# Performance work log

Hardware: AMD Instinct MI355X
Metric: run time of the kernel (lower is better)

Reference implementation:

```python
import jax, jax.numpy as jnp
import numpy as np

S, E, H, V = 2048, 1024, 1024, 32000


def setup_inputs() -> dict:
    key = jax.random.key(0)
    ks = jax.random.split(key, 12)
    def n(k, shape, s=0.02):
        return jax.random.normal(k, shape, dtype=jnp.float32) * s
    return {
        "encoder_out": n(ks[0], (S, E), 1.0),
        "word_input": jax.random.randint(ks[1], (1,), 0, V),
        "last_context": n(ks[2], (1, H), 1.0),
        "h0": jnp.zeros((1, 1, H), jnp.float32),
        "c0": jnp.zeros((1, 1, H), jnp.float32),
        "emb": n(ks[3], (V, E)),
        "W_ih": n(ks[4], (4 * H, E + H)),
        "b_ih": jnp.zeros((4 * H,), jnp.float32),
        "W_hh": n(ks[5], (4 * H, H)),
        "b_hh": jnp.zeros((4 * H,), jnp.float32),
        "W_att": n(ks[6], (H, E + H)),
        "b_att": jnp.zeros((H,), jnp.float32),
        "v": jax.random.uniform(ks[7], (H,), dtype=jnp.float32) * 0.1,
        "W_ah": n(ks[8], (H, E + H)),
        "b_ah": jnp.zeros((H,), jnp.float32),
        "W_out": n(ks[9], (V, H)),
        "b_out": jnp.zeros((V,), jnp.float32),
    }


def reference(encoder_out, word_input, last_context, h0, c0, emb,
              W_ih, b_ih, W_hh, b_hh, W_att, b_att, v, W_ah, b_ah,
              W_out, b_out):
    # --- single LSTM step (torch gate order: i, f, g, o) ---
    x_emb = emb[word_input[0]]                         # [E]
    lstm_in = jnp.concatenate([last_context[0], x_emb])  # [E+H]
    gates = W_ih @ lstm_in + b_ih + W_hh @ h0[0, 0] + b_hh  # [4H]
    i, f, g, o = jnp.split(gates, 4)
    i = jax.nn.sigmoid(i); f = jax.nn.sigmoid(f)
    g = jnp.tanh(g);       o = jax.nn.sigmoid(o)
    c = f * c0[0, 0] + i * g                           # [H]
    h = o * jnp.tanh(c)                                # [H] (dropout: eval = identity)

    # --- batched additive (Bahdanau-style) attention over all S steps ---
    cat = jnp.concatenate([jnp.broadcast_to(h[None, :], (S, H)), encoder_out], axis=1)  # [S, H+E]
    scores = jnp.tanh(cat @ W_att.T + b_att) @ v       # [S]
    w = jax.nn.softmax(scores)                         # [S]
    context = w @ encoder_out                          # [E]

    # --- output projection ---
    x_t = jnp.tanh(W_ah @ jnp.concatenate([context, h]) + b_ah)  # [H]
    output = jax.nn.log_softmax(W_out @ x_t + b_out)[None, :]    # [1, V]
    return (output, (h[None, None, :], c[None, None, :]), x_t[None, :], w[None, :])
```

## Files before the change

### kernel.cpp

```cpp
#include <hip/hip_runtime.h>
#include <math.h>

typedef unsigned short u16;
typedef unsigned int u32;

typedef float  floatx4 __attribute__((ext_vector_type(4)));
typedef short  shortx8 __attribute__((ext_vector_type(8)));

#define S_LEN 2048
#define E_DIM 1024
#define H_DIM 1024
#define V_DIM 32000

#define OUT_LOG 0
#define OUT_H   32000
#define OUT_C   33024
#define OUT_XT  34048
#define OUT_W   35072

#define WS_UB     0
#define WS_SCORES 1024
#define WS_CTX    3072
#define WS_EXPSUM 4097

__device__ __forceinline__ u16 f2bf_fast(float f) {
    union { float f; u32 i; } v; v.f = f;
    return (u16)((v.i + 0x8000u) >> 16);
}
__device__ __forceinline__ float red16_sum(float x) {
    #pragma unroll
    for (int m = 1; m <= 8; m <<= 1) x += __shfl_xor(x, m, 64);
    return x;
}
__device__ __forceinline__ float wave_sum(float x) {
    #pragma unroll
    for (int m = 32; m >= 1; m >>= 1) x += __shfl_xor(x, m, 64);
    return x;
}
__device__ __forceinline__ float wave_max(float x) {
    #pragma unroll
    for (int m = 32; m >= 1; m >>= 1) x = fmaxf(x, __shfl_xor(x, m, 64));
    return x;
}
__device__ __forceinline__ float dot4(float4 a, float4 b) {
    return a.x * b.x + a.y * b.y + a.z * b.z + a.w * b.w;
}
__device__ __forceinline__ void cvt8(u16* t, float4 a, float4 b) {
    t[0] = f2bf_fast(a.x); t[1] = f2bf_fast(a.y);
    t[2] = f2bf_fast(a.z); t[3] = f2bf_fast(a.w);
    t[4] = f2bf_fast(b.x); t[5] = f2bf_fast(b.y);
    t[6] = f2bf_fast(b.z); t[7] = f2bf_fast(b.w);
}

__global__ __launch_bounds__(256) void k_lstm(
    const float* __restrict__ last_ctx, const int* __restrict__ word,
    const float* __restrict__ emb, const float* __restrict__ h0,
    const float* __restrict__ c0,
    const float* __restrict__ W_ih, const float* __restrict__ b_ih,
    const float* __restrict__ W_hh, const float* __restrict__ b_hh,
    float* __restrict__ out_h, float* __restrict__ out_c)
{
    __shared__ float gsh[4];
    int tid = threadIdx.x;
    int g = tid >> 6, l = tid & 63;
    int j = blockIdx.x;
    int row = g * H_DIM + j;
    const float* embrow = emb + (size_t)word[0] * E_DIM;
    const float* wrow = W_ih + (size_t)row * (E_DIM + H_DIM);
    const float* hrow = W_hh + (size_t)row * H_DIM;
    int c4 = l * 4;

    float s = 0.f;
    #pragma unroll
    for (int it = 0; it < 4; ++it) {
        int col = it * 256 + c4;
        s += dot4(*(const float4*)(wrow + col), *(const float4*)(last_ctx + col));
    }
    #pragma unroll
    for (int it = 0; it < 4; ++it) {
        int col = it * 256 + c4;
        s += dot4(*(const float4*)(wrow + 1024 + col), *(const float4*)(embrow + col));
    }
    #pragma unroll
    for (int it = 0; it < 4; ++it) {
        int col = it * 256 + c4;
        s += dot4(*(const float4*)(hrow + col), *(const float4*)(h0 + col));
    }
    s = wave_sum(s);
    if (l == 0) gsh[g] = s + b_ih[row] + b_hh[row];
    __syncthreads();
    if (tid == 0) {
        float gi = 1.f / (1.f + expf(-gsh[0]));
        float gf = 1.f / (1.f + expf(-gsh[1]));
        float gg = tanhf(gsh[2]);
        float go = 1.f / (1.f + expf(-gsh[3]));
        float c = gf * c0[j] + gi * gg;
        float h = go * tanhf(c);
        out_h[j] = h;
        out_c[j] = c;
    }
}

__global__ __launch_bounds__(256) void k_uproj(
    const float* __restrict__ W_att, const float* __restrict__ b_att,
    const float* __restrict__ out_h, float* __restrict__ wsf)
{
    int tid = threadIdx.x;
    int gid = blockIdx.x * 256 + tid;
    if (gid < S_LEN) wsf[WS_SCORES + gid] = 0.f;
    else if (gid < S_LEN + E_DIM) wsf[WS_CTX + gid - S_LEN] = 0.f;
    else if (gid == S_LEN + E_DIM) wsf[WS_EXPSUM] = 0.f;

    int w = tid >> 6, l = tid & 63;
    int r = blockIdx.x * 4 + w;
    const float* wrow = W_att + (size_t)r * (E_DIM + H_DIM);
    int c4 = l * 4;
    float s = 0.f;
    #pragma unroll
    for (int it = 0; it < 4; ++it) {
        int col = it * 256 + c4;
        s += dot4(*(const float4*)(wrow + col), *(const float4*)(out_h + col));
    }
    s = wave_sum(s);
    if (l == 0) wsf[WS_UB + r] = s + b_att[r];
}

#define LDS_P 40
__global__ __launch_bounds__(256) void k_att_scores(
    const float* __restrict__ enc, const float* __restrict__ W_att,
    const float* __restrict__ vvec, const float* __restrict__ ws_ub,
    float* __restrict__ ws_scores)
{
    __shared__ u16 lds_a[2][128 * LDS_P];
    __shared__ u16 lds_b[2][64 * LDS_P];

    int tid = threadIdx.x;
    int w = tid >> 6, l = tid & 63;
    int b = blockIdx.x;
    int s0 = (b & 15) * 128;
    int r0 = (b >> 4) * 64;
    int lrow = l & 15, lq = l >> 4;

    int arow = tid >> 1, acol = (tid & 1) * 16;
    int brow = tid >> 2, bcol = (tid & 3) * 8;
    const float* pa_base = enc + (size_t)(s0 + arow) * E_DIM + acol;
    const float* pb_base = W_att + (size_t)(r0 + brow) * (E_DIM + H_DIM) + H_DIM + bcol;

    floatx4 acc[2][4];
    #pragma unroll
    for (int sf = 0; sf < 2; ++sf)
        #pragma unroll
        for (int i = 0; i < 4; ++i) acc[sf][i] = (floatx4)0.f;

    {
        float4 a0 = *(const float4*)(pa_base);
        float4 a1 = *(const float4*)(pa_base + 4);
        float4 a2 = *(const float4*)(pa_base + 8);
        float4 a3 = *(const float4*)(pa_base + 12);
        float4 b0 = *(const float4*)(pb_base);
        float4 b1 = *(const float4*)(pb_base + 4);
        u16 t[16];
        cvt8(t, a0, a1); cvt8(t + 8, a2, a3);
        *(uint4*)&lds_a[0][arow * LDS_P + acol]     = *(uint4*)(t);
        *(uint4*)&lds_a[0][arow * LDS_P + acol + 8] = *(uint4*)(t + 8);
        u16 tb[8];
        cvt8(tb, b0, b1);
        *(uint4*)&lds_b[0][brow * LDS_P + bcol] = *(uint4*)(tb);
    }
    __syncthreads();

    int cur = 0;
    for (int kc = 0; kc < 32; ++kc) {
        float4 nA0, nA1, nA2, nA3, nB0, nB1;
        if (kc < 31) {
            const float* pa = pa_base + (kc + 1) * 32;
            nA0 = *(const float4*)(pa);
            nA1 = *(const float4*)(pa + 4);
            nA2 = *(const float4*)(pa + 8);
            nA3 = *(const float4*)(pa + 12);
            const float* pb = pb_base + (kc + 1) * 32;
            nB0 = *(const float4*)(pb);
            nB1 = *(const float4*)(pb + 4);
        }

        shortx8 afrag0 = *(const shortx8*)&lds_a[cur][(w * 32 + lrow) * LDS_P + lq * 8];
        shortx8 afrag1 = *(const shortx8*)&lds_a[cur][(w * 32 + 16 + lrow) * LDS_P + lq * 8];
        #pragma unroll
        for (int rc = 0; rc < 4; ++rc) {
            shortx8 bfrag = *(const shortx8*)&lds_b[cur][(rc * 16 + lrow) * LDS_P + lq * 8];
            acc[0][rc] = __builtin_amdgcn_mfma_f32_16x16x32_bf16(afrag0, bfrag, acc[0][rc], 0, 0, 0);
            acc[1][rc] = __builtin_amdgcn_mfma_f32_16x16x32_bf16(afrag1, bfrag, acc[1][rc], 0, 0, 0);
        }

        if (kc < 31) {
            int nb = cur ^ 1;
            u16 t[16];
            cvt8(t, nA0, nA1); cvt8(t + 8, nA2, nA3);
            *(uint4*)&lds_a[nb][arow * LDS_P + acol]     = *(uint4*)(t);
            *(uint4*)&lds_a[nb][arow * LDS_P + acol + 8] = *(uint4*)(t + 8);
            u16 tb[8];
            cvt8(tb, nB0, nB1);
            *(uint4*)&lds_b[nb][brow * LDS_P + bcol] = *(uint4*)(tb);
        }
        __syncthreads();
        cur ^= 1;
    }

    float part[2][4] = {{0.f,0.f,0.f,0.f},{0.f,0.f,0.f,0.f}};
    #pragma unroll
    for (int rc = 0; rc < 4; ++rc) {
        int r = r0 + rc * 16 + lrow;
        float ubr = ws_ub[r];
        float vr  = vvec[r];
        #pragma unroll
        for (int sf = 0; sf < 2; ++sf)
            #pragma unroll
            for (int reg = 0; reg < 4; ++reg)
                part[sf][reg] += tanhf(acc[sf][rc][reg] + ubr) * vr;
    }
    #pragma unroll
    for (int m = 1; m <= 8; m <<= 1)
        #pragma unroll
        for (int sf = 0; sf < 2; ++sf)
            #pragma unroll
            for (int reg = 0; reg < 4; ++reg)
                part[sf][reg] += __shfl_xor(part[sf][reg], m, 64);
    if (lrow == 0) {
        #pragma unroll
        for (int sf = 0; sf < 2; ++sf) {
            int sbase = s0 + w * 32 + sf * 16 + lq * 4;
            #pragma unroll
            for (int reg = 0; reg < 4; ++reg)
                atomicAdd(&ws_scores[sbase + reg], part[sf][reg]);
        }
    }
}

__global__ __launch_bounds__(256) void k_ctx(
    const float* __restrict__ enc, const float* __restrict__ ws_scores,
    float* __restrict__ out_w, float* __restrict__ ws_ctx)
{
    __shared__ float red[4];
    __shared__ float w_lds[16];
    __shared__ float bM, bS;
    int tid = threadIdx.x, b = blockIdx.x;

    float4 sa = *(const float4*)(ws_scores + tid * 8);
    float4 sb = *(const float4*)(ws_scores + tid * 8 + 4);
    float m = fmaxf(fmaxf(fmaxf(sa.x, sa.y), fmaxf(sa.z, sa.w)),
                    fmaxf(fmaxf(sb.x, sb.y), fmaxf(sb.z, sb.w)));
    m = wave_max(m);
    if ((tid & 63) == 0) red[tid >> 6] = m;
    __syncthreads();
    if (tid == 0) bM = fmaxf(fmaxf(red[0], red[1]), fmaxf(red[2], red[3]));
    __syncthreads();
    float M = bM;
    float e = expf(sa.x - M) + expf(sa.y - M) + expf(sa.z - M) + expf(sa.w - M)
            + expf(sb.x - M) + expf(sb.y - M) + expf(sb.z - M) + expf(sb.w - M);
    e = wave_sum(e);
    if ((tid & 63) == 0) red[tid >> 6] = e;
    __syncthreads();
    if (tid == 0) bS = red[0] + red[1] + red[2] + red[3];
    __syncthreads();
    float inv = 1.f / bS;

    int sbase = b * 16;
    if (tid < 16) {
        float wt = expf(ws_scores[sbase + tid] - M) * inv;
        w_lds[tid] = wt;
        out_w[sbase + tid] = wt;
    }
    __syncthreads();

    int e4 = tid * 4;
    float a0 = 0.f, a1 = 0.f, a2 = 0.f, a3 = 0.f;
    #pragma unroll 4
    for (int i = 0; i < 16; ++i) {
        float wt = w_lds[i];
        float4 ev = *(const float4*)(enc + (size_t)(sbase + i) * E_DIM + e4);
        a0 += wt * ev.x; a1 += wt * ev.y; a2 += wt * ev.z; a3 += wt * ev.w;
    }
    atomicAdd(&ws_ctx[e4 + 0], a0);
    atomicAdd(&ws_ctx[e4 + 1], a1);
    atomicAdd(&ws_ctx[e4 + 2], a2);
    atomicAdd(&ws_ctx[e4 + 3], a3);
}

__global__ __launch_bounds__(256) void k_xt(
    const float* __restrict__ W_ah, const float* __restrict__ b_ah,
    const float* __restrict__ ws_ctx, const float* __restrict__ out_h,
    float* __restrict__ out_xt)
{
    int tid = threadIdx.x;
    int w = tid >> 6, l = tid & 63;
    int r = blockIdx.x * 4 + w;
    const float* wrow = W_ah + (size_t)r * (E_DIM + H_DIM);
    int c4 = l * 4;
    float s = 0.f;
    #pragma unroll
    for (int it = 0; it < 4; ++it) {
        int col = it * 256 + c4;
        s += dot4(*(const float4*)(wrow + col), *(const float4*)(ws_ctx + col));
        s += dot4(*(const float4*)(wrow + 1024 + col), *(const float4*)(out_h + col));
    }
    s = wave_sum(s);
    if (l == 0) out_xt[r] = tanhf(s + b_ah[r]);
}

__global__ __launch_bounds__(256) void k_logits(
    const float* __restrict__ W_out, const float* __restrict__ b_out,
    const float* __restrict__ out_xt,
    float* __restrict__ out_log, float* __restrict__ ws_expsum)
{
    __shared__ float red[4];
    int tid = threadIdx.x;
    int w = tid >> 6, l = tid & 63;
    int sub = l >> 4, l16 = l & 15;
    int row = blockIdx.x * 16 + w * 4 + sub;
    const float* wrow = W_out + (size_t)row * H_DIM;
    int c4 = l16 * 4;
    float s = 0.f;
    #pragma unroll 4
    for (int it = 0; it < 16; ++it) {
        int col = it * 64 + c4;
        s += dot4(*(const float4*)(wrow + col), *(const float4*)(out_xt + col));
    }
    s = red16_sum(s);
    float lg = s + b_out[row];
    float e = 0.f;
    if (l16 == 0) { out_log[row] = lg; e = expf(lg); }
    e = wave_sum(e);
    if (l == 0) red[w] = e;
    __syncthreads();
    if (tid == 0)
        atomicAdd(ws_expsum, red[0] + red[1] + red[2] + red[3]);
}

__global__ __launch_bounds__(256) void k_writeout(
    const float* __restrict__ ws_expsum, float* __restrict__ out_log)
{
    int i = blockIdx.x * 256 + threadIdx.x;
    float lz = logf(ws_expsum[0]);
    out_log[i] = out_log[i] - lz;
}

extern "C" void kernel_launch(void* const* d_in, const int* in_sizes, int n_in,
                              void* d_out, int out_size, void* d_ws, size_t ws_size,
                              hipStream_t stream) {
    const float* enc      = (const float*)d_in[0];
    const int*   word     = (const int*)d_in[1];
    const float* last_ctx = (const float*)d_in[2];
    const float* h0       = (const float*)d_in[3];
    const float* c0       = (const float*)d_in[4];
    const float* emb      = (const float*)d_in[5];
    const float* W_ih     = (const float*)d_in[6];
    const float* b_ih     = (const float*)d_in[7];
    const float* W_hh     = (const float*)d_in[8];
    const float* b_hh     = (const float*)d_in[9];
    const float* W_att    = (const float*)d_in[10];
    const float* b_att    = (const float*)d_in[11];
    const float* vvec     = (const float*)d_in[12];
    const float* W_ah     = (const float*)d_in[13];
    const float* b_ah     = (const float*)d_in[14];
    const float* W_out    = (const float*)d_in[15];
    const float* b_out    = (const float*)d_in[16];

    float* wsf = (float*)d_ws;

    float* out     = (float*)d_out;
    float* out_log = out + OUT_LOG;
    float* out_h   = out + OUT_H;
    float* out_c   = out + OUT_C;
    float* out_xt  = out + OUT_XT;
    float* out_w   = out + OUT_W;

    k_lstm<<<1024, 256, 0, stream>>>(last_ctx, word, emb, h0, c0,
                                     W_ih, b_ih, W_hh, b_hh, out_h, out_c);
    k_uproj<<<256, 256, 0, stream>>>(W_att, b_att, out_h, wsf);
    k_att_scores<<<256, 256, 0, stream>>>(enc, W_att, vvec,
                                          wsf + WS_UB, wsf + WS_SCORES);
    k_ctx<<<128, 256, 0, stream>>>(enc, wsf + WS_SCORES, out_w, wsf + WS_CTX);
    k_xt<<<256, 256, 0, stream>>>(W_ah, b_ah, wsf + WS_CTX, out_h, out_xt);
    k_logits<<<2000, 256, 0, stream>>>(W_out, b_out, out_xt,
                                       out_log, wsf + WS_EXPSUM);
    k_writeout<<<125, 256, 0, stream>>>(wsf + WS_EXPSUM, out_log);
}
```

Before: 373.5 us.

## Pre-convert encoder and W_att slices to bf16 in uproj kernel before MFMA scores

The fp32-to-bf16 conversion of encoder_out and the encoder half of W_att moves into the k_uproj kernel, which writes compact bf16 copies to workspace. The attention-score GEMM then loads bf16 directly into LDS. Before, each tile was re-read in fp32 and re-converted by all 16 (or 16) blocks that share it. This halves GEMM load bytes and removes the conversion ALU from the MFMA loop, at the cost of an extra fp32 read plus bf16 write pass in k_uproj.

```diff
diff --git a/kernel.cpp b/kernel.cpp
--- a/kernel.cpp
+++ b/kernel.cpp
@@ -22,6 +22,8 @@
 #define WS_SCORES 1024
 #define WS_CTX    3072
 #define WS_EXPSUM 4097
+#define WS_ENC16  4608
+#define WS_W16    (4608 + 1048576)
 
 __device__ __forceinline__ u16 f2bf_fast(float f) {
     union { float f; u32 i; } v; v.f = f;
@@ -103,16 +105,18 @@
 
 __global__ __launch_bounds__(256) void k_uproj(
     const float* __restrict__ W_att, const float* __restrict__ b_att,
-    const float* __restrict__ out_h, float* __restrict__ wsf)
+    const float* __restrict__ out_h, const float* __restrict__ enc,
+    float* __restrict__ wsf)
 {
     int tid = threadIdx.x;
-    int gid = blockIdx.x * 256 + tid;
+    int b = blockIdx.x;
+    int gid = b * 256 + tid;
     if (gid < S_LEN) wsf[WS_SCORES + gid] = 0.f;
     else if (gid < S_LEN + E_DIM) wsf[WS_CTX + gid - S_LEN] = 0.f;
     else if (gid == S_LEN + E_DIM) wsf[WS_EXPSUM] = 0.f;
 
     int w = tid >> 6, l = tid & 63;
-    int r = blockIdx.x * 4 + w;
+    int r = b * 4 + w;
     const float* wrow = W_att + (size_t)r * (E_DIM + H_DIM);
     int c4 = l * 4;
     float s = 0.f;
@@ -123,11 +127,43 @@
     }
     s = wave_sum(s);
     if (l == 0) wsf[WS_UB + r] = s + b_att[r];
+
+    u16* enc16 = (u16*)(wsf + WS_ENC16);
+    u16* w16   = (u16*)(wsf + WS_W16);
+    {
+        int row = b * 8 + (tid >> 5);
+        int col = (tid & 31) * 32;
+        const float* src = enc + (size_t)row * E_DIM + col;
+        u16 t[32];
+        #pragma unroll
+        for (int m = 0; m < 32; m += 8) {
+            float4 x = *(const float4*)(src + m);
+            float4 y = *(const float4*)(src + m + 4);
+            cvt8(t + m, x, y);
+        }
+        uint4* dst = (uint4*)(enc16 + (size_t)row * E_DIM + col);
+        #pragma unroll
+        for (int m = 0; m < 4; ++m) dst[m] = *(uint4*)(t + m * 8);
+    }
+    {
+        int row = b * 4 + (tid >> 6);
+        int col = (tid & 63) * 16;
+        const float* src = W_att + (size_t)row * (E_DIM + H_DIM) + H_DIM + col;
+        u16 t[16];
+        float4 x0 = *(const float4*)(src);
+        float4 x1 = *(const float4*)(src + 4);
+        float4 x2 = *(const float4*)(src + 8);
+        float4 x3 = *(const float4*)(src + 12);
+        cvt8(t, x0, x1); cvt8(t + 8, x2, x3);
+        uint4* dst = (uint4*)(w16 + (size_t)row * E_DIM + col);
+        dst[0] = *(uint4*)(t);
+        dst[1] = *(uint4*)(t + 8);
+    }
 }
 
 #define LDS_P 40
 __global__ __launch_bounds__(256) void k_att_scores(
-    const float* __restrict__ enc, const float* __restrict__ W_att,
+    const u16* __restrict__ enc16, const u16* __restrict__ w16,
     const float* __restrict__ vvec, const float* __restrict__ ws_ub,
     float* __restrict__ ws_scores)
 {
@@ -143,8 +179,8 @@
 
     int arow = tid >> 1, acol = (tid & 1) * 16;
     int brow = tid >> 2, bcol = (tid & 3) * 8;
-    const float* pa_base = enc + (size_t)(s0 + arow) * E_DIM + acol;
-    const float* pb_base = W_att + (size_t)(r0 + brow) * (E_DIM + H_DIM) + H_DIM + bcol;
+    const u16* pa_base = enc16 + (size_t)(s0 + arow) * E_DIM + acol;
+    const u16* pb_base = w16 + (size_t)(r0 + brow) * E_DIM + bcol;
 
     floatx4 acc[2][4];
     #pragma unroll
@@ -153,34 +189,23 @@
         for (int i = 0; i < 4; ++i) acc[sf][i] = (floatx4)0.f;
 
     {
-        float4 a0 = *(const float4*)(pa_base);
-        float4 a1 = *(const float4*)(pa_base + 4);
-        float4 a2 = *(const float4*)(pa_base + 8);
-        float4 a3 = *(const float4*)(pa_base + 12);
-        float4 b0 = *(const float4*)(pb_base);
-        float4 b1 = *(const float4*)(pb_base + 4);
-        u16 t[16];
-        cvt8(t, a0, a1); cvt8(t + 8, a2, a3);
-        *(uint4*)&lds_a[0][arow * LDS_P + acol]     = *(uint4*)(t);
-        *(uint4*)&lds_a[0][arow * LDS_P + acol + 8] = *(uint4*)(t + 8);
-        u16 tb[8];
-        cvt8(tb, b0, b1);
-        *(uint4*)&lds_b[0][brow * LDS_P + bcol] = *(uint4*)(tb);
+        uint4 a0 = *(const uint4*)(pa_base);
+        uint4 a1 = *(const uint4*)(pa_base + 8);
+        uint4 b0 = *(const uint4*)(pb_base);
+        *(uint4*)&lds_a[0][arow * LDS_P + acol]     = a0;
+        *(uint4*)&lds_a[0][arow * LDS_P + acol + 8] = a1;
+        *(uint4*)&lds_b[0][brow * LDS_P + bcol]     = b0;
     }
     __syncthreads();
 
     int cur = 0;
     for (int kc = 0; kc < 32; ++kc) {
-        float4 nA0, nA1, nA2, nA3, nB0, nB1;
+        uint4 nA0, nA1, nB0;
         if (kc < 31) {
-            const float* pa = pa_base + (kc + 1) * 32;
-            nA0 = *(const float4*)(pa);
-            nA1 = *(const float4*)(pa + 4);
-            nA2 = *(const float4*)(pa + 8);
-            nA3 = *(const float4*)(pa + 12);
-            const float* pb = pb_base + (kc + 1) * 32;
-            nB0 = *(const float4*)(pb);
-            nB1 = *(const float4*)(pb + 4);
+            const u16* pa = pa_base + (kc + 1) * 32;
+            nA0 = *(const uint4*)(pa);
+            nA1 = *(const uint4*)(pa + 8);
+            nB0 = *(const uint4*)(pb_base + (kc + 1) * 32);
         }
 
         shortx8 afrag0 = *(const shortx8*)&lds_a[cur][(w * 32 + lrow) * LDS_P + lq * 8];
@@ -194,13 +219,9 @@
 
         if (kc < 31) {
             int nb = cur ^ 1;
-            u16 t[16];
-            cvt8(t, nA0, nA1); cvt8(t + 8, nA2, nA3);
-            *(uint4*)&lds_a[nb][arow * LDS_P + acol]     = *(uint4*)(t);
-            *(uint4*)&lds_a[nb][arow * LDS_P + acol + 8] = *(uint4*)(t + 8);
-            u16 tb[8];
-            cvt8(tb, nB0, nB1);
-            *(uint4*)&lds_b[nb][brow * LDS_P + bcol] = *(uint4*)(tb);
+            *(uint4*)&lds_a[nb][arow * LDS_P + acol]     = nA0;
+            *(uint4*)&lds_a[nb][arow * LDS_P + acol + 8] = nA1;
+            *(uint4*)&lds_b[nb][brow * LDS_P + bcol]     = nB0;
         }
         __syncthreads();
         cur ^= 1;
@@ -376,9 +397,10 @@
 
     k_lstm<<<1024, 256, 0, stream>>>(last_ctx, word, emb, h0, c0,
                                      W_ih, b_ih, W_hh, b_hh, out_h, out_c);
-    k_uproj<<<256, 256, 0, stream>>>(W_att, b_att, out_h, wsf);
-    k_att_scores<<<256, 256, 0, stream>>>(enc, W_att, vvec,
-                                          wsf + WS_UB, wsf + WS_SCORES);
+    k_uproj<<<256, 256, 0, stream>>>(W_att, b_att, out_h, enc, wsf);
+    k_att_scores<<<256, 256, 0, stream>>>((const u16*)(wsf + WS_ENC16),
+                                          (const u16*)(wsf + WS_W16),
+                                          vvec, wsf + WS_UB, wsf + WS_SCORES);
     k_ctx<<<128, 256, 0, stream>>>(enc, wsf + WS_SCORES, out_w, wsf + WS_CTX);
     k_xt<<<256, 256, 0, stream>>>(W_ah, b_ah, wsf + WS_CTX, out_h, out_xt);
     k_logits<<<2000, 256, 0, stream>>>(W_out, b_out, out_xt,
```

After: 362.7 us. -2.9%, faster.
